# Kernel optimization log

Hardware: AMD Instinct MI355X
Metric: run time of the kernel (lower is better)

## Reference

```python
import jax, jax.numpy as jnp
import numpy as np

EMBED_DIM = 1024
NUM_HEADS = 16
HEAD_DIM = EMBED_DIM // NUM_HEADS


def setup_inputs() -> dict:
    key = jax.random.key(0)
    k1, k2, k3, k4, k5 = jax.random.split(key, 5)
    B, S, D = 1, 4096, EMBED_DIM
    scale = 0.02
    return {
        "input": jax.random.normal(k1, (B, S, D), dtype=jnp.float32),
        "Wqkv": jax.random.normal(k2, (D, 3 * D), dtype=jnp.float32) * scale,
        "bqkv": jax.random.normal(k3, (3 * D,), dtype=jnp.float32) * scale,
        "Wo": jax.random.normal(k4, (D, D), dtype=jnp.float32) * scale,
        "bo": jax.random.normal(k5, (D,), dtype=jnp.float32) * scale,
    }


def reference(input, Wqkv, bqkv, Wo, bo):
    B, S, D = input.shape
    H, Hd = NUM_HEADS, HEAD_DIM
    qkv = input @ Wqkv + bqkv                        # [B, S, 3D]
    qkv = qkv.reshape(B, S, 3, H, Hd)
    qkv = jnp.transpose(qkv, (2, 0, 3, 1, 4))        # [3, B, H, S, Hd]
    q, k, v = qkv[0], qkv[1], qkv[2]
    scores = jnp.einsum("bhsd,bhtd->bhst", q, k) / (Hd ** 0.5)  # [B,H,S,S]
    causal = jnp.tril(jnp.ones((S, S), dtype=bool))[None, None]
    scores = jnp.where(causal, scores, -jnp.inf)
    attn = jax.nn.softmax(scores, axis=-1)
    out = jnp.einsum("bhst,bhtd->bhsd", attn, v)     # [B,H,S,Hd]
    out = jnp.transpose(out, (0, 2, 1, 3)).reshape(B, S, D)
    return out @ Wo + bo
```

## Files before the change

### kernel.cpp

```cpp
#include <hip/hip_runtime.h>

typedef __bf16 bf16;
typedef __bf16 bf16x8 __attribute__((ext_vector_type(8)));
typedef float f32x4 __attribute__((ext_vector_type(4)));
typedef float f32x16 __attribute__((ext_vector_type(16)));
typedef unsigned u32x2 __attribute__((ext_vector_type(2)));

#define MFMA16(a, b, c) __builtin_amdgcn_mfma_f32_16x16x32_bf16((a), (b), (c), 0, 0, 0)
#define MFMA32(a, b, c) __builtin_amdgcn_mfma_f32_32x32x16_bf16((a), (b), (c), 0, 0, 0)

typedef const __attribute__((address_space(1))) uint32_t glb_u32;
typedef __attribute__((address_space(3))) uint32_t lds_u32;
#define GLOAD16(gp, lp) __builtin_amdgcn_global_load_lds((glb_u32*)(gp), (lds_u32*)(lp), 16, 0, 0)

__global__ __launch_bounds__(256) void k_prep(const float* __restrict__ X, bf16* __restrict__ Xb,
                                              const float* __restrict__ Wqkv, bf16* __restrict__ WqkvT,
                                              const float* __restrict__ Wo, bf16* __restrict__ WoT) {
    __shared__ float tile[64][65];
    int bid = blockIdx.x;
    int t = threadIdx.x;
    if (bid < 2048) {
        size_t i = ((size_t)bid * 256 + t) * 8;
        float4 a = *(const float4*)(X + i);
        float4 b = *(const float4*)(X + i + 4);
        bf16 e[8];
        e[0] = (bf16)a.x; e[1] = (bf16)a.y; e[2] = (bf16)a.z; e[3] = (bf16)a.w;
        e[4] = (bf16)b.x; e[5] = (bf16)b.y; e[6] = (bf16)b.z; e[7] = (bf16)b.w;
        uint4 u; __builtin_memcpy(&u, e, 16);
        *(uint4*)(Xb + i) = u;
        return;
    }
    const float* in; bf16* out; int R, C, bx, by;
    if (bid < 2816) {
        in = Wqkv; out = WqkvT; R = 1024; C = 3072;
        int b = bid - 2048; bx = b % 48; by = b / 48;
    } else {
        in = Wo; out = WoT; R = 1024; C = 1024;
        int b = bid - 2816; bx = b & 15; by = b >> 4;
    }
    for (int i = 0; i < 16; ++i) {
        int e = i * 256 + t; int r = e >> 6, c = e & 63;
        tile[r][c] = in[(size_t)(by * 64 + r) * C + bx * 64 + c];
    }
    __syncthreads();
    for (int i = 0; i < 16; ++i) {
        int e = i * 256 + t; int r = e >> 6, c = e & 63;
        out[(size_t)(bx * 64 + r) * R + by * 64 + c] = (bf16)tile[c][r];
    }
}

__device__ __forceinline__ void gemm128_core(const bf16* __restrict__ A, const bf16* __restrict__ Bt,
                                             int r0, int c0, int Kd, char* As, char* Bs,
                                             f32x4 (&acc)[4][4]) {
    int t = threadIdx.x, l = t & 63, w = t >> 6;
    int g = l >> 4, li = l & 15;
    int wr = w >> 1, wc = w & 1;
    for (int k0 = 0; k0 < Kd; k0 += 64) {
        __syncthreads();
        #pragma unroll
        for (int i = 0; i < 4; ++i) {
            int slot = i * 256 + t;
            int row = slot >> 3;
            int ch  = (slot & 7) ^ (row & 7);
            int base = (i * 256 + w * 64) * 16;
            GLOAD16(A  + (size_t)(r0 + row) * Kd + k0 + ch * 8, As + base);
            GLOAD16(Bt + (size_t)(c0 + row) * Kd + k0 + ch * 8, Bs + base);
        }
        __syncthreads();
        __builtin_amdgcn_s_setprio(1);
        #pragma unroll
        for (int kk = 0; kk < 2; ++kk) {
            bf16x8 af[4], bfr[4];
            #pragma unroll
            for (int m = 0; m < 4; ++m) {
                int row = wr * 64 + m * 16 + li;
                af[m] = *(const bf16x8*)(As + ((row * 128 + kk * 64 + g * 16) ^ ((row & 7) << 4)));
            }
            #pragma unroll
            for (int n = 0; n < 4; ++n) {
                int row = wc * 64 + n * 16 + li;
                bfr[n] = *(const bf16x8*)(Bs + ((row * 128 + kk * 64 + g * 16) ^ ((row & 7) << 4)));
            }
            #pragma unroll
            for (int m = 0; m < 4; ++m)
                #pragma unroll
                for (int n = 0; n < 4; ++n)
                    acc[m][n] = MFMA16(af[m], bfr[n], acc[m][n]);
        }
        __builtin_amdgcn_s_setprio(0);
    }
}

__global__ __launch_bounds__(256) void k_gemm_qkv(const bf16* __restrict__ Xb, const bf16* __restrict__ WqkvT,
                                                  const float* __restrict__ bqkv,
                                                  bf16* __restrict__ Q, bf16* __restrict__ Kfr,
                                                  bf16* __restrict__ Vfr) {
    __shared__ __align__(16) char As[16384];
    __shared__ __align__(16) char Bs[16384];
    int bid = blockIdx.x;
    int Lg = (bid & 7) * 96 + (bid >> 3);
    int bx = Lg % 24, by = Lg / 24;
    int r0 = by * 128, c0 = bx * 128;
    f32x4 acc[4][4] = {};
    gemm128_core(Xb, WqkvT, r0, c0, 1024, As, Bs, acc);
    int t = threadIdx.x, l = t & 63, w = t >> 6;
    int g = l >> 4, li = l & 15;
    int wr = w >> 1, wc = w & 1;
    int colbase = c0 + wc * 64;
    int sec = colbase >> 10;
    int head = (colbase & 1023) >> 6;
    if (sec == 0) {
        const float scale = 0.125f * 1.44269504f;
        #pragma unroll
        for (int m = 0; m < 4; ++m)
            #pragma unroll
            for (int n = 0; n < 4; ++n) {
                int hd = n * 16 + li;
                float bias = bqkv[colbase + hd];
                #pragma unroll
                for (int r = 0; r < 4; ++r) {
                    int row = r0 + wr * 64 + m * 16 + g * 4 + r;
                    Q[(size_t)(head * 4096 + row) * 64 + hd] = (bf16)((acc[m][n][r] + bias) * scale);
                }
            }
    } else if (sec == 1) {
        bf16* dstK = Kfr + (size_t)head * 262144;
        #pragma unroll
        for (int m = 0; m < 4; ++m) {
            int tbase = r0 + wr * 64 + m * 16 + g * 4;
            size_t tpart = (size_t)(tbase >> 5) * 2048 + (size_t)(tbase & 31) * 8;
            #pragma unroll
            for (int n = 0; n < 4; ++n) {
                int hd = n * 16 + li;
                float bias = bqkv[colbase + hd];
                size_t A0 = tpart + (size_t)(hd >> 4) * 512 + (size_t)((hd >> 3) & 1) * 256 + (hd & 7);
                #pragma unroll
                for (int r = 0; r < 4; ++r)
                    dstK[A0 + (size_t)r * 8] = (bf16)(acc[m][n][r] + bias);
            }
        }
    } else {
        bf16* dstV = Vfr + (size_t)head * 262144;
        #pragma unroll
        for (int m = 0; m < 4; ++m) {
            int tbase = r0 + wr * 64 + m * 16 + g * 4;
            size_t tpart = (size_t)(tbase >> 5) * 2048 + (size_t)((tbase >> 4) & 1) * 512
                         + (size_t)((tbase >> 3) & 1) * 256 + (tbase & 7);
            #pragma unroll
            for (int n = 0; n < 4; ++n) {
                int hd = n * 16 + li;
                float bias = bqkv[colbase + hd];
                size_t A0 = tpart + (size_t)(hd >> 5) * 1024 + (size_t)(hd & 31) * 8;
                bf16 e4[4];
                #pragma unroll
                for (int r = 0; r < 4; ++r) e4[r] = (bf16)(acc[m][n][r] + bias);
                unsigned long long pk; __builtin_memcpy(&pk, e4, 8);
                *(unsigned long long*)(dstV + A0) = pk;
            }
        }
    }
}

__global__ __launch_bounds__(256) void k_gemm_out(const bf16* __restrict__ Ob, const bf16* __restrict__ WoT,
                                                  const float* __restrict__ bo, float* __restrict__ out) {
    __shared__ __align__(16) char As[16384];
    __shared__ __align__(16) char Bs[8192];
    int bid = blockIdx.x;
    int Lg = (bid & 7) * 64 + (bid >> 3);
    int bx = Lg & 15, by = Lg >> 4;
    int r0 = by * 128, c0 = bx * 64;
    int t = threadIdx.x, l = t & 63, w = t >> 6;
    int g = l >> 4, li = l & 15;
    f32x4 acc[2][4] = {};
    for (int k0 = 0; k0 < 1024; k0 += 64) {
        __syncthreads();
        #pragma unroll
        for (int i = 0; i < 4; ++i) {
            int slot = i * 256 + t;
            int row = slot >> 3;
            int ch  = (slot & 7) ^ (row & 7);
            int base = (i * 256 + w * 64) * 16;
            GLOAD16(Ob + (size_t)(r0 + row) * 1024 + k0 + ch * 8, As + base);
        }
        #pragma unroll
        for (int i = 0; i < 2; ++i) {
            int slot = i * 256 + t;
            int row = slot >> 3;
            int ch  = (slot & 7) ^ (row & 7);
            int base = (i * 256 + w * 64) * 16;
            GLOAD16(WoT + (size_t)(c0 + row) * 1024 + k0 + ch * 8, Bs + base);
        }
        __syncthreads();
        __builtin_amdgcn_s_setprio(1);
        #pragma unroll
        for (int kk = 0; kk < 2; ++kk) {
            bf16x8 af[2], bfr[4];
            #pragma unroll
            for (int m = 0; m < 2; ++m) {
                int row = w * 32 + m * 16 + li;
                af[m] = *(const bf16x8*)(As + ((row * 128 + kk * 64 + g * 16) ^ ((row & 7) << 4)));
            }
            #pragma unroll
            for (int n = 0; n < 4; ++n) {
                int row = n * 16 + li;
                bfr[n] = *(const bf16x8*)(Bs + ((row * 128 + kk * 64 + g * 16) ^ ((row & 7) << 4)));
            }
            #pragma unroll
            for (int m = 0; m < 2; ++m)
                #pragma unroll
                for (int n = 0; n < 4; ++n)
                    acc[m][n] = MFMA16(af[m], bfr[n], acc[m][n]);
        }
        __builtin_amdgcn_s_setprio(0);
    }
    #pragma unroll
    for (int m = 0; m < 2; ++m)
        #pragma unroll
        for (int n = 0; n < 4; ++n) {
            int col = c0 + n * 16 + li;
            float bias = bo[col];
            #pragma unroll
            for (int r = 0; r < 4; ++r) {
                int row = r0 + w * 32 + m * 16 + g * 4 + r;
                out[(size_t)row * 1024 + col] = acc[m][n][r] + bias;
            }
        }
}

__device__ __forceinline__ unsigned pkbf(float a, float b) {
    bf16 h0 = (bf16)a, h1 = (bf16)b;
    unsigned short u0, u1;
    __builtin_memcpy(&u0, &h0, 2); __builtin_memcpy(&u1, &h1, 2);
    return (unsigned)u0 | ((unsigned)u1 << 16);
}

__global__ __launch_bounds__(128) void k_attn(const bf16* __restrict__ Q, const uint4* __restrict__ Kfr,
                                              const uint4* __restrict__ Vfr, bf16* __restrict__ O) {
    __shared__ float Op[32][64];
    __shared__ float Ml[2][32];
    int bid = blockIdx.x;
    int h = bid & 15;
    int u = bid >> 4;
    int jj = (u < 64) ? u : 191 - u;
    int w = threadIdx.x >> 6;
    int l = threadIdx.x & 63;
    int lc = l & 31, hi = l >> 5;
    int hi4 = hi * 4, hi8 = hi * 8;
    const bf16* Qh = Q + (size_t)h * 4096 * 64;
    const uint4* Kh = Kfr + (size_t)h * 32768;
    const uint4* Vh = Vfr + (size_t)h * 32768;
    int nt = jj + 1;
    int hA = (nt + 1) >> 1;
    int tb = w ? hA : 0;
    int te = w ? nt : hA;

    f32x16 oacc[2] = {};
    float m = -1e30f, lsum = 0.f;
    uint4 kA[4], vA[4], kB[4], vB[4];
    bf16x8 qf[4];
    #pragma unroll
    for (int kst = 0; kst < 4; ++kst)
        qf[kst] = *(const bf16x8*)(Qh + (size_t)(jj * 32 + lc) * 64 + kst * 16 + hi8);

    auto compute = [&](int tt, uint4 (&kf)[4], uint4 (&vf)[4]) {
        f32x16 sacc = {};
        __builtin_amdgcn_s_setprio(1);
        #pragma unroll
        for (int kst = 0; kst < 4; ++kst) {
            bf16x8 kk; __builtin_memcpy(&kk, &kf[kst], 16);
            sacc = MFMA32(kk, qf[kst], sacc);
        }
        __builtin_amdgcn_s_setprio(0);
        if (tt == jj) {
            #pragma unroll
            for (int r = 0; r < 16; ++r) {
                int tloc = (r & 3) + 8 * (r >> 2) + hi4;
                if (tloc > lc) sacc[r] = -1e30f;
            }
        }
        float t8[8];
        #pragma unroll
        for (int r = 0; r < 8; ++r) t8[r] = fmaxf(sacc[r], sacc[r + 8]);
        float ta = fmaxf(fmaxf(t8[0], t8[1]), t8[2]);
        float tb3 = fmaxf(fmaxf(t8[3], t8[4]), t8[5]);
        float tc = fmaxf(t8[6], t8[7]);
        float pm = fmaxf(fmaxf(ta, tb3), tc);
        pm = fmaxf(pm, __shfl_xor(pm, 32));
        if (!__all(pm - m <= 8.0f)) {
            float mn = fmaxf(m, pm);
            float al = exp2f(m - mn);
            #pragma unroll
            for (int r = 0; r < 16; ++r) {
                int ql = (r & 3) + 8 * (r >> 2) + hi4;
                float alb = __shfl(al, ql);
                oacc[0][r] *= alb;
                oacc[1][r] *= alb;
            }
            lsum *= al;
            m = mn;
        }
        float pv[16];
        float rs0 = 0.f, rs1 = 0.f;
        #pragma unroll
        for (int r = 0; r < 8; ++r) {
            pv[r]     = exp2f(sacc[r] - m);     rs0 += pv[r];
            pv[r + 8] = exp2f(sacc[r + 8] - m); rs1 += pv[r + 8];
        }
        lsum += rs0 + rs1;
        #pragma unroll
        for (int ks = 0; ks < 2; ++ks) {
            int b = ks * 8;
            unsigned a0 = pkbf(pv[b + 0], pv[b + 1]), a1 = pkbf(pv[b + 2], pv[b + 3]);
            unsigned b0 = pkbf(pv[b + 4], pv[b + 5]), b1 = pkbf(pv[b + 6], pv[b + 7]);
            u32x2 r0 = __builtin_amdgcn_permlane32_swap(a0, b0, false, false);
            u32x2 r1 = __builtin_amdgcn_permlane32_swap(a1, b1, false, false);
            unsigned wsq[4] = { r0[0], r1[0], r0[1], r1[1] };
            bf16x8 pa; __builtin_memcpy(&pa, wsq, 16);
            __builtin_amdgcn_s_setprio(1);
            #pragma unroll
            for (int jt = 0; jt < 2; ++jt) {
                bf16x8 vv; __builtin_memcpy(&vv, &vf[jt * 2 + ks], 16);
                oacc[jt] = MFMA32(pa, vv, oacc[jt]);
            }
            __builtin_amdgcn_s_setprio(0);
        }
    };

    if (te > tb) {
        #pragma unroll
        for (int i = 0; i < 4; ++i) {
            kA[i] = Kh[(size_t)tb * 256 + i * 64 + l];
            vA[i] = Vh[(size_t)tb * 256 + i * 64 + l];
        }
        int i = tb;
        for (; i + 2 <= te; i += 2) {
            const uint4* Kn = Kh + (size_t)(i + 1) * 256;
            const uint4* Vn = Vh + (size_t)(i + 1) * 256;
            #pragma unroll
            for (int q = 0; q < 4; ++q) { kB[q] = Kn[q * 64 + l]; vB[q] = Vn[q * 64 + l]; }
            compute(i, kA, vA);
            if (i + 2 < te) {
                const uint4* K2 = Kh + (size_t)(i + 2) * 256;
                const uint4* V2 = Vh + (size_t)(i + 2) * 256;
                #pragma unroll
                for (int q = 0; q < 4; ++q) { kA[q] = K2[q * 64 + l]; vA[q] = V2[q * 64 + l]; }
            }
            compute(i + 1, kB, vB);
        }
        if ((te - tb) & 1) compute(te - 1, kA, vA);
    }
    lsum += __shfl_xor(lsum, 32);

    if (w == 1) {
        #pragma unroll
        for (int r = 0; r < 16; ++r) {
            int ql = (r & 3) + 8 * (r >> 2) + hi4;
            Op[ql][lc]      = oacc[0][r];
            Op[ql][32 + lc] = oacc[1][r];
        }
        if (hi == 0) { Ml[0][lc] = m; Ml[1][lc] = lsum; }
    }
    __syncthreads();
    if (w == 0) {
        float mo = Ml[0][lc], lo = Ml[1][lc];
        float mm = fmaxf(m, mo);
        float alr = exp2f(m - mm), alo = exp2f(mo - mm);
        float lf = lsum * alr + lo * alo;
        float inv = 1.0f / lf;
        float fr = alr * inv, fo = alo * inv;
        int q0 = jj * 32;
        #pragma unroll
        for (int r = 0; r < 16; ++r) {
            int ql = (r & 3) + 8 * (r >> 2) + hi4;
            float frb = __shfl(fr, ql), fob = __shfl(fo, ql);
            float o0 = oacc[0][r] * frb + Op[ql][lc]      * fob;
            float o1 = oacc[1][r] * frb + Op[ql][32 + lc] * fob;
            int row = q0 + ql;
            O[(size_t)row * 1024 + h * 64 + lc]      = (bf16)o0;
            O[(size_t)row * 1024 + h * 64 + 32 + lc] = (bf16)o1;
        }
    }
}

extern "C" void kernel_launch(void* const* d_in, const int* in_sizes, int n_in,
                              void* d_out, int out_size, void* d_ws, size_t ws_size,
                              hipStream_t stream) {
    const float* X    = (const float*)d_in[0];
    const float* Wqkv = (const float*)d_in[1];
    const float* bqkv = (const float*)d_in[2];
    const float* Wo   = (const float*)d_in[3];
    const float* bo   = (const float*)d_in[4];
    float* out = (float*)d_out;

    char* ws = (char*)d_ws;
    const size_t MB = 1024 * 1024;
    bf16*  Xb    = (bf16*)(ws);
    bf16*  WqkvT = (bf16*)(ws + 8  * MB);
    bf16*  WoT   = (bf16*)(ws + 14 * MB);
    bf16*  Qb    = (bf16*)(ws + 16 * MB);
    uint4* Kfr   = (uint4*)(ws + 40 * MB);
    uint4* Vfr   = (uint4*)(ws + 48 * MB);
    bf16*  Ob    = Xb;

    k_prep<<<3072, 256, 0, stream>>>(X, Xb, Wqkv, WqkvT, Wo, WoT);
    k_gemm_qkv<<<768, 256, 0, stream>>>(Xb, WqkvT, bqkv, Qb, (bf16*)Kfr, (bf16*)Vfr);
    k_attn<<<2048, 128, 0, stream>>>(Qb, Kfr, Vfr, Ob);
    k_gemm_out<<<512, 256, 0, stream>>>(Ob, WoT, bo, out);
}
```

Measured before the change: 147.8 us.

## Split attention KV halves into separate blocks with a merge kernel

```diff
diff --git a/kernel.cpp b/kernel.cpp
--- a/kernel.cpp
+++ b/kernel.cpp
@@ -234,16 +234,16 @@
     return (unsigned)u0 | ((unsigned)u1 << 16);
 }
 
-__global__ __launch_bounds__(128) void k_attn(const bf16* __restrict__ Q, const uint4* __restrict__ Kfr,
-                                              const uint4* __restrict__ Vfr, bf16* __restrict__ O) {
-    __shared__ float Op[32][64];
-    __shared__ float Ml[2][32];
+__global__ __launch_bounds__(64) void k_attn(const bf16* __restrict__ Q, const uint4* __restrict__ Kfr,
+                                             const uint4* __restrict__ Vfr,
+                                             bf16* __restrict__ Opart, float* __restrict__ Mlp) {
     int bid = blockIdx.x;
     int h = bid & 15;
-    int u = bid >> 4;
-    int jj = (u < 64) ? u : 191 - u;
-    int w = threadIdx.x >> 6;
-    int l = threadIdx.x & 63;
+    int r2 = bid >> 4;
+    int s = r2 >> 7;
+    int p = r2 & 127;
+    int jj = (p < 64) ? p : 191 - p;
+    int l = threadIdx.x;
     int lc = l & 31, hi = l >> 5;
     int hi4 = hi * 4, hi8 = hi * 8;
     const bf16* Qh = Q + (size_t)h * 4096 * 64;
@@ -251,8 +251,8 @@
     const uint4* Vh = Vfr + (size_t)h * 32768;
     int nt = jj + 1;
     int hA = (nt + 1) >> 1;
-    int tb = w ? hA : 0;
-    int te = w ? nt : hA;
+    int tb = s ? hA : 0;
+    int te = s ? nt : hA;
 
     f32x16 oacc[2] = {};
     float m = -1e30f, lsum = 0.f;
@@ -351,34 +351,50 @@
     }
     lsum += __shfl_xor(lsum, 32);
 
-    if (w == 1) {
-        #pragma unroll
-        for (int r = 0; r < 16; ++r) {
-            int ql = (r & 3) + 8 * (r >> 2) + hi4;
-            Op[ql][lc]      = oacc[0][r];
-            Op[ql][32 + lc] = oacc[1][r];
-        }
-        if (hi == 0) { Ml[0][lc] = m; Ml[1][lc] = lsum; }
-    }
-    __syncthreads();
-    if (w == 0) {
-        float mo = Ml[0][lc], lo = Ml[1][lc];
-        float mm = fmaxf(m, mo);
-        float alr = exp2f(m - mm), alo = exp2f(mo - mm);
-        float lf = lsum * alr + lo * alo;
-        float inv = 1.0f / lf;
-        float fr = alr * inv, fo = alo * inv;
-        int q0 = jj * 32;
-        #pragma unroll
-        for (int r = 0; r < 16; ++r) {
-            int ql = (r & 3) + 8 * (r >> 2) + hi4;
-            float frb = __shfl(fr, ql), fob = __shfl(fo, ql);
-            float o0 = oacc[0][r] * frb + Op[ql][lc]      * fob;
-            float o1 = oacc[1][r] * frb + Op[ql][32 + lc] * fob;
-            int row = q0 + ql;
-            O[(size_t)row * 1024 + h * 64 + lc]      = (bf16)o0;
-            O[(size_t)row * 1024 + h * 64 + 32 + lc] = (bf16)o1;
-        }
+    int idx = (h * 128 + jj) * 2 + s;
+    bf16* op = Opart + (size_t)idx * 2048;
+    #pragma unroll
+    for (int r = 0; r < 16; ++r) {
+        int ql = (r & 3) + 8 * (r >> 2) + hi4;
+        op[ql * 64 + lc]      = (bf16)oacc[0][r];
+        op[ql * 64 + 32 + lc] = (bf16)oacc[1][r];
+    }
+    if (hi == 0) {
+        Mlp[(size_t)idx * 64 + lc]      = m;
+        Mlp[(size_t)idx * 64 + 32 + lc] = lsum;
+    }
+}
+
+__global__ __launch_bounds__(64) void k_attn_merge(const bf16* __restrict__ Opart,
+                                                   const float* __restrict__ Mlp,
+                                                   bf16* __restrict__ O) {
+    int bid = blockIdx.x;
+    int h = bid & 15;
+    int jj = bid >> 4;
+    int idx0 = (h * 128 + jj) * 2;
+    int l = threadIdx.x;
+    int r = l >> 1, half = l & 1;
+    float m0 = Mlp[(size_t)idx0 * 64 + r],       l0 = Mlp[(size_t)idx0 * 64 + 32 + r];
+    float m1 = Mlp[(size_t)(idx0 + 1) * 64 + r], l1 = Mlp[(size_t)(idx0 + 1) * 64 + 32 + r];
+    float mm = fmaxf(m0, m1);
+    float e0 = exp2f(m0 - mm), e1 = exp2f(m1 - mm);
+    float inv = 1.0f / (l0 * e0 + l1 * e1);
+    float w0 = e0 * inv, w1 = e1 * inv;
+    const bf16* p0 = Opart + (size_t)idx0 * 2048 + r * 64 + half * 32;
+    const bf16* p1 = p0 + 2048;
+    bf16* dst = O + (size_t)(jj * 32 + r) * 1024 + h * 64 + half * 32;
+    #pragma unroll
+    for (int i = 0; i < 4; ++i) {
+        uint4 a = *(const uint4*)(p0 + i * 8);
+        uint4 b = *(const uint4*)(p1 + i * 8);
+        bf16 ea[8], eb[8], eo[8];
+        __builtin_memcpy(ea, &a, 16);
+        __builtin_memcpy(eb, &b, 16);
+        #pragma unroll
+        for (int j = 0; j < 8; ++j)
+            eo[j] = (bf16)((float)ea[j] * w0 + (float)eb[j] * w1);
+        uint4 o; __builtin_memcpy(&o, eo, 16);
+        *(uint4*)(dst + i * 8) = o;
     }
 }
 
@@ -398,12 +414,15 @@
     bf16*  WqkvT = (bf16*)(ws + 8  * MB);
     bf16*  WoT   = (bf16*)(ws + 14 * MB);
     bf16*  Qb    = (bf16*)(ws + 16 * MB);
+    bf16*  Opart = (bf16*)(ws + 24 * MB);
     uint4* Kfr   = (uint4*)(ws + 40 * MB);
     uint4* Vfr   = (uint4*)(ws + 48 * MB);
+    float* Mlp   = (float*)(ws + 8 * MB);
     bf16*  Ob    = Xb;
 
     k_prep<<<3072, 256, 0, stream>>>(X, Xb, Wqkv, WqkvT, Wo, WoT);
     k_gemm_qkv<<<768, 256, 0, stream>>>(Xb, WqkvT, bqkv, Qb, (bf16*)Kfr, (bf16*)Vfr);
-    k_attn<<<2048, 128, 0, stream>>>(Qb, Kfr, Vfr, Ob);
+    k_attn<<<4096, 64, 0, stream>>>(Qb, Kfr, Vfr, Opart, Mlp);
+    k_attn_merge<<<2048, 64, 0, stream>>>(Opart, Mlp, Ob);
     k_gemm_out<<<512, 256, 0, stream>>>(Ob, WoT, bo, out);
 }
```

Result: slower. 162.9 us (+10.3%).
